# Kernel optimization log

Hardware: AMD Instinct MI355X
Metric: run time of the kernel (lower is better)

Reference implementation:

```python
import jax, jax.numpy as jnp
import numpy as np

D_MODEL = 1024; D_STATE = 128; D_CONV = 4; EXPAND = 2; HEADDIM = 64
D_INNER = EXPAND * D_MODEL          # 2048
NHEADS = D_INNER // HEADDIM         # 32
CONV_DIM = D_INNER + 2 * D_STATE    # 2304 (ngroups=1)
D_IN_PROJ = 2 * D_INNER + 2 * D_STATE + NHEADS  # 4384
B = 2; L = 2048; EPS = 1e-5


def _rmsnorm(x, w):
    return x * jax.lax.rsqrt(jnp.mean(x * x, axis=-1, keepdims=True) + EPS) * w


def _mamba2(x, W_in, conv_w, conv_b, dt_bias, A_log, Dskip, norm_w, W_out):
    # Faithful Mamba2 forward (mamba-ssm defaults: ngroups=1, rmsnorm gated, no proj bias)
    Bb, Ll, _ = x.shape
    zxbcdt = x @ W_in.T                                   # (B,L,D_IN_PROJ)
    z = zxbcdt[..., :D_INNER]
    xBC = zxbcdt[..., D_INNER:D_INNER + CONV_DIM]
    dt = jax.nn.softplus(zxbcdt[..., D_INNER + CONV_DIM:] + dt_bias)  # (B,L,H)
    # depthwise causal conv1d + silu over xBC
    xBC = jnp.transpose(xBC, (0, 2, 1))                   # (B,C,L)
    xBC = jax.lax.conv_general_dilated(xBC, conv_w[:, None, :], (1,), [(D_CONV - 1, 0)],
                                       feature_group_count=CONV_DIM)
    xBC = jax.nn.silu(jnp.transpose(xBC + conv_b[None, :, None], (0, 2, 1)))  # (B,L,C)
    xs = xBC[..., :D_INNER].reshape(Bb, Ll, NHEADS, HEADDIM)
    Bm = xBC[..., D_INNER:D_INNER + D_STATE]              # (B,L,N)
    Cm = xBC[..., D_INNER + D_STATE:]                     # (B,L,N)
    A = -jnp.exp(A_log)                                   # (H,)
    dA = jnp.exp(dt * A)                                  # (B,L,H)

    def step(state, inp):
        dA_t, dt_t, B_t, C_t, x_t = inp
        dBx = jnp.einsum('bh,bn,bhp->bhpn', dt_t, B_t, x_t)
        state = state * dA_t[:, :, None, None] + dBx      # (B,H,P,N)
        return state, jnp.einsum('bhpn,bn->bhp', state, C_t)

    state0 = jnp.zeros((Bb, NHEADS, HEADDIM, D_STATE), x.dtype)
    _, y = jax.lax.scan(step, state0,
                        (jnp.moveaxis(dA, 1, 0), jnp.moveaxis(dt, 1, 0), jnp.moveaxis(Bm, 1, 0),
                         jnp.moveaxis(Cm, 1, 0), jnp.moveaxis(xs, 1, 0)))
    y = jnp.moveaxis(y, 0, 1) + Dskip[None, None, :, None] * xs  # D skip connection
    y = y.reshape(Bb, Ll, D_INNER)
    y = _rmsnorm(y * jax.nn.silu(z), norm_w)              # gated RMSNorm
    return y @ W_out.T                                    # (B,L,D_MODEL)


def setup_inputs() -> dict:
    key = jax.random.key(0)
    ks = jax.random.split(key, 4)

    def nrm(k, shape, s=0.02):
        return jax.random.normal(k, shape, jnp.float32) * s

    def mamba_params(kk):
        k = jax.random.split(kk, 5)
        return dict(W_in=nrm(k[0], (D_IN_PROJ, D_MODEL)),
                    conv_w=nrm(k[1], (CONV_DIM, D_CONV), 0.2),
                    conv_b=jnp.zeros((CONV_DIM,), jnp.float32),
                    dt_bias=jax.random.uniform(k[2], (NHEADS,), jnp.float32, -4.0, -2.0),
                    A_log=jnp.log(jax.random.uniform(k[3], (NHEADS,), jnp.float32, 1.0, 16.0)),
                    D=jnp.ones((NHEADS,), jnp.float32),
                    norm_w=jnp.ones((D_INNER,), jnp.float32),
                    W_out=nrm(k[4], (D_MODEL, D_INNER)))

    pf = mamba_params(ks[1]); pb = mamba_params(ks[2])
    out = {"x": jax.random.normal(ks[0], (B, L, D_MODEL), jnp.float32),
           "norm_weight": jnp.ones((D_MODEL,), jnp.float32)}
    out.update({f"fwd_{k}": v for k, v in pf.items()})
    out.update({f"bwd_{k}": v for k, v in pb.items()})
    out["proj_W"] = nrm(ks[3], (D_MODEL, 2 * D_MODEL))
    out["proj_b"] = jnp.zeros((D_MODEL,), jnp.float32)
    return out


def reference(x, norm_weight,
              fwd_W_in, fwd_conv_w, fwd_conv_b, fwd_dt_bias, fwd_A_log, fwd_D, fwd_norm_w, fwd_W_out,
              bwd_W_in, bwd_conv_w, bwd_conv_b, bwd_dt_bias, bwd_A_log, bwd_D, bwd_norm_w, bwd_W_out,
              proj_W, proj_b):
    residual = x
    xn = _rmsnorm(x, norm_weight)
    y_fwd = _mamba2(xn, fwd_W_in, fwd_conv_w, fwd_conv_b, fwd_dt_bias, fwd_A_log, fwd_D, fwd_norm_w, fwd_W_out)
    y_bwd = jnp.flip(_mamba2(jnp.flip(xn, 1), bwd_W_in, bwd_conv_w, bwd_conv_b, bwd_dt_bias,
                             bwd_A_log, bwd_D, bwd_norm_w, bwd_W_out), 1)
    out = jnp.concatenate([y_fwd, y_bwd], axis=-1) @ proj_W.T + proj_b
    return residual + out
```

## Files before the change

kernel.cpp:

```cpp
#include <hip/hip_runtime.h>
#include <math.h>

#define B_ 2
#define L_ 2048
#define DM 1024
#define DS 128
#define DI 2048
#define NH 32
#define CONVD 2304
#define DIP 4384
#define NPAD 4480
#define EPS_ 1e-5f
#define Q_ 128
#define NC_ 16
#define PT 136

typedef __attribute__((ext_vector_type(8))) short bf16x8;
typedef __attribute__((ext_vector_type(4))) float f32x4;

__device__ __forceinline__ float silu_f(float x) { return x / (1.0f + __expf(-x)); }

__device__ __forceinline__ unsigned short f2bf(float x) {
    union { float f; unsigned u; } v; v.f = x;
    unsigned r = v.u + 0x7fffu + ((v.u >> 16) & 1u);
    return (unsigned short)(r >> 16);
}
__device__ __forceinline__ float bf2f(unsigned short s) {
    union { unsigned u; float f; } v; v.u = ((unsigned)s) << 16; return v.f;
}

__device__ __forceinline__ void gload_lds16(const unsigned short* g, unsigned short* l) {
    __builtin_amdgcn_global_load_lds(
        (const __attribute__((address_space(1))) unsigned int*)g,
        (__attribute__((address_space(3))) unsigned int*)l, 16, 0, 0);
}

__global__ __launch_bounds__(256) void castpad_kernel(
    const float* __restrict__ src, unsigned short* __restrict__ dst, int n_src, int n_dst)
{
    int i = (blockIdx.x * 256 + threadIdx.x) * 4;
    if (i >= n_dst) return;
    ushort4 o;
    if (i < n_src) {
        float4 v = *(const float4*)(src + i);
        o = make_ushort4(f2bf(v.x), f2bf(v.y), f2bf(v.z), f2bf(v.w));
    } else {
        o = make_ushort4(0, 0, 0, 0);
    }
    *(ushort4*)(dst + i) = o;
}

__global__ __launch_bounds__(256) void rmsnorm_kernel(
    const float* __restrict__ x, const float* __restrict__ w, unsigned short* __restrict__ out)
{
    int row = blockIdx.x;
    int t = threadIdx.x;
    const float4* xr = (const float4*)(x + (size_t)row * DM);
    float4 v = xr[t];
    float ss = v.x*v.x + v.y*v.y + v.z*v.z + v.w*v.w;
#pragma unroll
    for (int o = 32; o > 0; o >>= 1) ss += __shfl_down(ss, o, 64);
    __shared__ float red[4];
    if ((t & 63) == 0) red[t >> 6] = ss;
    __syncthreads();
    float tot = red[0] + red[1] + red[2] + red[3];
    float inv = rsqrtf(tot * (1.0f / DM) + EPS_);
    float4 wv = ((const float4*)w)[t];
    ushort4 o4 = make_ushort4(f2bf(v.x * inv * wv.x), f2bf(v.y * inv * wv.y),
                              f2bf(v.z * inv * wv.z), f2bf(v.w * inv * wv.w));
    ((ushort4*)(out + (size_t)row * DM))[t] = o4;
}

__global__ __launch_bounds__(256, 2) void gemm_bf16_kernel(
    const unsigned short* __restrict__ A, const unsigned short* __restrict__ Wt,
    float* __restrict__ C, unsigned short* __restrict__ C16,
    const float* __restrict__ bias, const float* __restrict__ resid,
    int M, int N, int K, int ldc, int col_off, int flipA, int flipOut)
{
    __shared__ unsigned short As[128 * 32];
    __shared__ unsigned short Bs[128 * 32];
    const int tid = threadIdx.x;
    const int lane = tid & 63, wave = tid >> 6;
    const int wr = wave >> 1, wc = wave & 1;
    const int r16 = lane & 15, kg = lane >> 4;
    const int bn0 = blockIdx.x * 128;
    const int bm0 = blockIdx.y * 128;

    f32x4 acc[4][4];
#pragma unroll
    for (int m = 0; m < 4; ++m)
#pragma unroll
        for (int n = 0; n < 4; ++n) { f32x4 z = {0.f, 0.f, 0.f, 0.f}; acc[m][n] = z; }

    for (int k0 = 0; k0 < K; k0 += 32) {
#pragma unroll
        for (int i = 0; i < 2; ++i) {
            int c = wave * 128 + i * 64 + lane;
            int r = c >> 2;
            int kk = (c & 3) << 3;
            int gr = bm0 + r;
            if (flipA) gr ^= (L_ - 1);
            gload_lds16(A + (size_t)gr * K + k0 + kk, As + (size_t)(wave * 128 + i * 64) * 8);
            gload_lds16(Wt + (size_t)(bn0 + r) * K + k0 + kk, Bs + (size_t)(wave * 128 + i * 64) * 8);
        }
        __syncthreads();
        bf16x8 af[4], bfr[4];
        const bf16x8* Ap = (const bf16x8*)As;
        const bf16x8* Bp = (const bf16x8*)Bs;
#pragma unroll
        for (int m = 0; m < 4; ++m) af[m] = Ap[(wr * 64 + m * 16 + r16) * 4 + kg];
#pragma unroll
        for (int n = 0; n < 4; ++n) bfr[n] = Bp[(wc * 64 + n * 16 + r16) * 4 + kg];
#pragma unroll
        for (int m = 0; m < 4; ++m)
#pragma unroll
            for (int n = 0; n < 4; ++n)
                acc[m][n] = __builtin_amdgcn_mfma_f32_16x16x32_bf16(af[m], bfr[n], acc[m][n], 0, 0, 0);
        __syncthreads();
    }

#pragma unroll
    for (int m = 0; m < 4; ++m) {
        int row = bm0 + wr * 64 + m * 16 + kg * 4;
#pragma unroll
        for (int n = 0; n < 4; ++n) {
            int col = bn0 + wc * 64 + n * 16 + r16;
            if (col < N) {
                float bv = bias ? bias[col] : 0.f;
#pragma unroll
                for (int j = 0; j < 4; ++j) {
                    int ro = flipOut ? ((row + j) ^ (L_ - 1)) : (row + j);
                    size_t o = (size_t)ro * ldc + col_off + col;
                    float val = acc[m][n][j] + bv;
                    if (resid) val += resid[o];
                    if (C16) C16[o] = f2bf(val);
                    else     C[o] = val;
                }
            }
        }
    }
}

__global__ __launch_bounds__(256) void convdt_kernel(
    const float* __restrict__ zx, const float* __restrict__ conv_w,
    const float* __restrict__ conv_b, const float* __restrict__ dt_bias,
    const float* __restrict__ A_log,
    float* __restrict__ xs, float* __restrict__ bc,
    float* __restrict__ dtb, float* __restrict__ dab)
{
    int row = blockIdx.x;
    int l = row & (L_ - 1);
    int t = threadIdx.x;
#pragma unroll
    for (int cc = 0; cc < 9; ++cc) {
        int c = t + cc * 256;
        float acc = conv_b[c];
#pragma unroll
        for (int k = 0; k < 4; ++k) {
            int ll = l - 3 + k;
            if (ll >= 0)
                acc = fmaf(conv_w[c * 4 + k], zx[(size_t)(row - 3 + k) * DIP + DI + c], acc);
        }
        float v = silu_f(acc);
        if (c < DI) xs[(size_t)row * DI + c] = v;
        else        bc[(size_t)row * (2 * DS) + (c - DI)] = v;
    }
    if (t < NH) {
        float xv = zx[(size_t)row * DIP + DI + CONVD + t] + dt_bias[t];
        float dt = (xv > 20.f) ? xv : log1pf(__expf(xv));
        float a = -__expf(A_log[t]);
        dtb[row * NH + t] = dt;
        dab[row * NH + t] = dt * a;
    }
}

__global__ __launch_bounds__(256) void chunk_state_kernel(
    const float* __restrict__ xs, const float* __restrict__ bc,
    const float* __restrict__ dtb, const float* __restrict__ dab,
    float* __restrict__ scs, float* __restrict__ la_sum)
{
    int bh = blockIdx.x, c = blockIdx.y;
    int b = bh >> 5, h = bh & 31;
    size_t base = (size_t)b * L_ + (size_t)c * Q_;
    int t = threadIdx.x;
    const int lane = t & 63, wave = t >> 6;
    const int r16 = lane & 15, kg = lane >> 4;
    const int wr = wave >> 1, wc = wave & 1;

    __shared__ unsigned short xwT[64 * PT];
    __shared__ unsigned short BT[128 * PT];
    __shared__ float la[128], w[128];

    if (t < 128) la[t] = dab[(base + t) * NH + h];
    __syncthreads();
#pragma unroll
    for (int off = 1; off < 128; off <<= 1) {
        float v = 0.f;
        if (t < 128 && t >= off) v = la[t - off];
        __syncthreads();
        if (t < 128) la[t] += v;
        __syncthreads();
    }
    float ltot = la[127];
    if (t < 128) w[t] = __expf(ltot - la[t]) * dtb[(base + t) * NH + h];
    if (t == 0) la_sum[bh * NC_ + c] = ltot;
    __syncthreads();

#pragma unroll
    for (int i = 0; i < 8; ++i) {
        int lin4 = i * 256 + t;
        int s = lin4 >> 4, p4 = (lin4 & 15) << 2;
        float4 xv = *(const float4*)&xs[(base + s) * DI + h * 64 + p4];
        float ws = w[s];
        xwT[(p4 + 0) * PT + s] = f2bf(xv.x * ws);
        xwT[(p4 + 1) * PT + s] = f2bf(xv.y * ws);
        xwT[(p4 + 2) * PT + s] = f2bf(xv.z * ws);
        xwT[(p4 + 3) * PT + s] = f2bf(xv.w * ws);
    }
#pragma unroll
    for (int i = 0; i < 16; ++i) {
        int lin4 = i * 256 + t;
        int s = lin4 >> 5, n4 = (lin4 & 31) << 2;
        float4 bv = *(const float4*)&bc[(base + s) * (2 * DS) + n4];
        BT[(n4 + 0) * PT + s] = f2bf(bv.x);
        BT[(n4 + 1) * PT + s] = f2bf(bv.y);
        BT[(n4 + 2) * PT + s] = f2bf(bv.z);
        BT[(n4 + 3) * PT + s] = f2bf(bv.w);
    }
    __syncthreads();

    f32x4 acc[2][4];
#pragma unroll
    for (int m = 0; m < 2; ++m)
#pragma unroll
        for (int n = 0; n < 4; ++n) { f32x4 z = {0.f, 0.f, 0.f, 0.f}; acc[m][n] = z; }

#pragma unroll
    for (int ks = 0; ks < 4; ++ks) {
        bf16x8 af[2], bfr[4];
#pragma unroll
        for (int m = 0; m < 2; ++m)
            af[m] = *(const bf16x8*)&xwT[(wr * 32 + m * 16 + r16) * PT + ks * 32 + kg * 8];
#pragma unroll
        for (int n = 0; n < 4; ++n)
            bfr[n] = *(const bf16x8*)&BT[(wc * 64 + n * 16 + r16) * PT + ks * 32 + kg * 8];
#pragma unroll
        for (int m = 0; m < 2; ++m)
#pragma unroll
            for (int n = 0; n < 4; ++n)
                acc[m][n] = __builtin_amdgcn_mfma_f32_16x16x32_bf16(af[m], bfr[n], acc[m][n], 0, 0, 0);
    }

    float* outp = scs + (size_t)(bh * NC_ + c) * 8192;
#pragma unroll
    for (int m = 0; m < 2; ++m) {
        int p0 = wr * 32 + m * 16 + kg * 4;
#pragma unroll
        for (int n = 0; n < 4; ++n) {
            int nn = wc * 64 + n * 16 + r16;
#pragma unroll
            for (int j = 0; j < 4; ++j)
                outp[(p0 + j) * 128 + nn] = acc[m][n][j];
        }
    }
}

__global__ __launch_bounds__(256) void chunk_seq_kernel(
    float* __restrict__ scs, const float* __restrict__ la_sum)
{
    int bh = blockIdx.x, t = threadIdx.x;
    float S[32];
#pragma unroll
    for (int i = 0; i < 32; ++i) S[i] = 0.f;
    for (int c = 0; c < NC_; ++c) {
        float ef = __expf(la_sum[bh * NC_ + c]);
        float* p = scs + (size_t)(bh * NC_ + c) * 8192;
#pragma unroll
        for (int i = 0; i < 32; ++i) {
            int idx = i * 256 + t;
            float tmp = p[idx];
            p[idx] = S[i];
            S[i] = fmaf(S[i], ef, tmp);
        }
    }
}

__global__ __launch_bounds__(256) void chunk_out_kernel(
    const float* __restrict__ xs, const float* __restrict__ bc,
    const float* __restrict__ dtb, const float* __restrict__ dab,
    const float* __restrict__ scs, const float* __restrict__ Dskip,
    float* __restrict__ ys)
{
    int bh = blockIdx.x, c = blockIdx.y;
    int b = bh >> 5, h = bh & 31;
    size_t base = (size_t)b * L_ + (size_t)c * Q_;
    int t = threadIdx.x;
    const int lane = t & 63, wave = t >> 6;
    const int r16 = lane & 15, kg = lane >> 4;

    __shared__ unsigned short Cb[128 * PT];
    __shared__ unsigned short Bb[128 * PT];
    __shared__ unsigned short xTb[64 * PT];
    __shared__ unsigned short Sinb[64 * PT];
    __shared__ float la[128], dt[128];

    if (t < 128) {
        la[t] = dab[(base + t) * NH + h];
        dt[t] = dtb[(base + t) * NH + h];
    }
    __syncthreads();
#pragma unroll
    for (int off = 1; off < 128; off <<= 1) {
        float v = 0.f;
        if (t < 128 && t >= off) v = la[t - off];
        __syncthreads();
        if (t < 128) la[t] += v;
        __syncthreads();
    }

#pragma unroll
    for (int i = 0; i < 16; ++i) {
        int lin4 = i * 256 + t;
        int s = lin4 >> 5, n4 = (lin4 & 31) << 2;
        float4 bv = *(const float4*)&bc[(base + s) * (2 * DS) + n4];
        float4 cv = *(const float4*)&bc[(base + s) * (2 * DS) + 128 + n4];
        *(ushort4*)&Bb[s * PT + n4] = make_ushort4(f2bf(bv.x), f2bf(bv.y), f2bf(bv.z), f2bf(bv.w));
        *(ushort4*)&Cb[s * PT + n4] = make_ushort4(f2bf(cv.x), f2bf(cv.y), f2bf(cv.z), f2bf(cv.w));
    }
#pragma unroll
    for (int i = 0; i < 8; ++i) {
        int lin4 = i * 256 + t;
        int s = lin4 >> 4, p4 = (lin4 & 15) << 2;
        float4 xv = *(const float4*)&xs[(base + s) * DI + h * 64 + p4];
        xTb[(p4 + 0) * PT + s] = f2bf(xv.x);
        xTb[(p4 + 1) * PT + s] = f2bf(xv.y);
        xTb[(p4 + 2) * PT + s] = f2bf(xv.z);
        xTb[(p4 + 3) * PT + s] = f2bf(xv.w);
    }
    {
        const float* sin_g = scs + (size_t)(bh * NC_ + c) * 8192;
#pragma unroll
        for (int i = 0; i < 8; ++i) {
            int lin4 = i * 256 + t;
            int p = lin4 >> 5, n4 = (lin4 & 31) << 2;
            float4 sv = *(const float4*)&sin_g[p * 128 + n4];
            *(ushort4*)&Sinb[p * PT + n4] = make_ushort4(f2bf(sv.x), f2bf(sv.y), f2bf(sv.z), f2bf(sv.w));
        }
    }
    __syncthreads();

    const int wr = wave >> 1, wc = wave & 1;
    f32x4 acc[4][4];
#pragma unroll
    for (int m = 0; m < 4; ++m)
#pragma unroll
        for (int n = 0; n < 4; ++n) { f32x4 z = {0.f, 0.f, 0.f, 0.f}; acc[m][n] = z; }
    const bool skipq = (wr == 0 && wc == 1);
    if (!skipq) {
#pragma unroll
        for (int ks = 0; ks < 4; ++ks) {
            bf16x8 af[4], bfr[4];
#pragma unroll
            for (int m = 0; m < 4; ++m)
                af[m] = *(const bf16x8*)&Cb[(wr * 64 + m * 16 + r16) * PT + ks * 32 + kg * 8];
#pragma unroll
            for (int n = 0; n < 4; ++n)
                bfr[n] = *(const bf16x8*)&Bb[(wc * 64 + n * 16 + r16) * PT + ks * 32 + kg * 8];
#pragma unroll
            for (int m = 0; m < 4; ++m)
#pragma unroll
                for (int n = 0; n < 4; ++n)
                    acc[m][n] = __builtin_amdgcn_mfma_f32_16x16x32_bf16(af[m], bfr[n], acc[m][n], 0, 0, 0);
        }
    }
    __syncthreads();

#pragma unroll
    for (int m = 0; m < 4; ++m) {
        int t0 = wr * 64 + m * 16 + kg * 4;
#pragma unroll
        for (int n = 0; n < 4; ++n) {
            int sx = wc * 64 + n * 16 + r16;
            float las = la[sx], dts = dt[sx];
#pragma unroll
            for (int j = 0; j < 4; ++j) {
                int tr = t0 + j;
                float v = 0.f;
                if (!skipq && sx <= tr) v = acc[m][n][j] * __expf(la[tr] - las) * dts;
                Bb[tr * PT + sx] = f2bf(v);
            }
        }
    }

    const int wr2 = wave >> 1, wc2 = wave & 1;
    f32x4 acc2[4][2];
#pragma unroll
    for (int m = 0; m < 4; ++m)
#pragma unroll
        for (int n = 0; n < 2; ++n) { f32x4 z = {0.f, 0.f, 0.f, 0.f}; acc2[m][n] = z; }
#pragma unroll
    for (int ks = 0; ks < 4; ++ks) {
        bf16x8 af[4], bfr[2];
#pragma unroll
        for (int m = 0; m < 4; ++m)
            af[m] = *(const bf16x8*)&Cb[(wr2 * 64 + m * 16 + r16) * PT + ks * 32 + kg * 8];
#pragma unroll
        for (int n = 0; n < 2; ++n)
            bfr[n] = *(const bf16x8*)&Sinb[(wc2 * 32 + n * 16 + r16) * PT + ks * 32 + kg * 8];
#pragma unroll
        for (int m = 0; m < 4; ++m)
#pragma unroll
            for (int n = 0; n < 2; ++n)
                acc2[m][n] = __builtin_amdgcn_mfma_f32_16x16x32_bf16(af[m], bfr[n], acc2[m][n], 0, 0, 0);
    }
#pragma unroll
    for (int m = 0; m < 4; ++m) {
        int t0 = wr2 * 64 + m * 16 + kg * 4;
#pragma unroll
        for (int j = 0; j < 4; ++j) {
            float e = __expf(la[t0 + j]);
#pragma unroll
            for (int n = 0; n < 2; ++n) acc2[m][n][j] *= e;
        }
    }
    __syncthreads();

#pragma unroll
    for (int ks = 0; ks < 4; ++ks) {
        bf16x8 af[4], bfr[2];
#pragma unroll
        for (int m = 0; m < 4; ++m)
            af[m] = *(const bf16x8*)&Bb[(wr2 * 64 + m * 16 + r16) * PT + ks * 32 + kg * 8];
#pragma unroll
        for (int n = 0; n < 2; ++n)
            bfr[n] = *(const bf16x8*)&xTb[(wc2 * 32 + n * 16 + r16) * PT + ks * 32 + kg * 8];
#pragma unroll
        for (int m = 0; m < 4; ++m)
#pragma unroll
            for (int n = 0; n < 2; ++n)
                acc2[m][n] = __builtin_amdgcn_mfma_f32_16x16x32_bf16(af[m], bfr[n], acc2[m][n], 0, 0, 0);
    }

    float Dv = Dskip[h];
#pragma unroll
    for (int m = 0; m < 4; ++m) {
        int t0 = wr2 * 64 + m * 16 + kg * 4;
#pragma unroll
        for (int n = 0; n < 2; ++n) {
            int p = wc2 * 32 + n * 16 + r16;
#pragma unroll
            for (int j = 0; j < 4; ++j) {
                int tr = t0 + j;
                float xv = bf2f(xTb[p * PT + tr]);
                ys[(base + tr) * DI + h * 64 + p] = acc2[m][n][j] + Dv * xv;
            }
        }
    }
}

__global__ __launch_bounds__(256) void gate_kernel(
    const float* __restrict__ ys, const float* __restrict__ zx,
    const float* __restrict__ nw, unsigned short* __restrict__ u)
{
    int row = blockIdx.x;
    int t = threadIdx.x;
    const float4* yr = (const float4*)(ys + (size_t)row * DI);
    const float4* zr = (const float4*)(zx + (size_t)row * DIP);
    float g[2][4];
    float ss = 0.f;
#pragma unroll
    for (int it = 0; it < 2; ++it) {
        int i = t + it * 256;
        float4 y4 = yr[i];
        float4 z4 = zr[i];
        float gv;
        gv = y4.x * silu_f(z4.x); g[it][0] = gv; ss += gv * gv;
        gv = y4.y * silu_f(z4.y); g[it][1] = gv; ss += gv * gv;
        gv = y4.z * silu_f(z4.z); g[it][2] = gv; ss += gv * gv;
        gv = y4.w * silu_f(z4.w); g[it][3] = gv; ss += gv * gv;
    }
#pragma unroll
    for (int o = 32; o > 0; o >>= 1) ss += __shfl_down(ss, o, 64);
    __shared__ float red[4];
    if ((t & 63) == 0) red[t >> 6] = ss;
    __syncthreads();
    float tot = red[0] + red[1] + red[2] + red[3];
    float inv = rsqrtf(tot * (1.0f / DI) + EPS_);
#pragma unroll
    for (int it = 0; it < 2; ++it) {
        int i = t + it * 256;
        float4 w4 = ((const float4*)nw)[i];
        ushort4 o4 = make_ushort4(f2bf(g[it][0] * inv * w4.x), f2bf(g[it][1] * inv * w4.y),
                                  f2bf(g[it][2] * inv * w4.z), f2bf(g[it][3] * inv * w4.w));
        ((ushort4*)(u + (size_t)row * DI))[i] = o4;
    }
}

extern "C" void kernel_launch(void* const* d_in, const int* in_sizes, int n_in,
                              void* d_out, int out_size, void* d_ws, size_t ws_size,
                              hipStream_t stream)
{
    (void)in_sizes; (void)n_in; (void)out_size;
    const float* x        = (const float*)d_in[0];
    const float* norm_w   = (const float*)d_in[1];
    const float* Win[2]   = {(const float*)d_in[2],  (const float*)d_in[10]};
    const float* convw[2] = {(const float*)d_in[3],  (const float*)d_in[11]};
    const float* convb[2] = {(const float*)d_in[4],  (const float*)d_in[12]};
    const float* dtbias[2]= {(const float*)d_in[5],  (const float*)d_in[13]};
    const float* Alog[2]  = {(const float*)d_in[6],  (const float*)d_in[14]};
    const float* Dsk[2]   = {(const float*)d_in[7],  (const float*)d_in[15]};
    const float* mnw[2]   = {(const float*)d_in[8],  (const float*)d_in[16]};
    const float* Wout[2]  = {(const float*)d_in[9],  (const float*)d_in[17]};
    const float* projW    = (const float*)d_in[18];
    const float* projb    = (const float*)d_in[19];
    float* out = (float*)d_out;

    const int M = B_ * L_;

    char* base = (char*)d_ws;
    size_t off = 0;
    #define WALLOC(name, type, count) \
        type* name = (type*)(base + off); off = (off + (size_t)(count) * sizeof(type) + 255) & ~(size_t)255;
    WALLOC(xnb,  unsigned short, (size_t)M * DM)
    WALLOC(zx,   float,          (size_t)M * DIP)
    WALLOC(xs,   float,          (size_t)M * DI)
    WALLOC(bcb,  float,          (size_t)M * 2 * DS)
    WALLOC(dtb,  float,          (size_t)M * NH)
    WALLOC(dab,  float,          (size_t)M * NH)
    WALLOC(ysb,  float,          (size_t)M * DI)
    WALLOC(ub,   unsigned short, (size_t)M * DI)
    WALLOC(dbb,  unsigned short, (size_t)M * DI)
    WALLOC(scs,  float,          (size_t)64 * NC_ * 64 * 128)
    WALLOC(lasum, float,         (size_t)64 * NC_)
    WALLOC(winb0, unsigned short, (size_t)NPAD * DM)
    WALLOC(winb1, unsigned short, (size_t)NPAD * DM)
    WALLOC(woutb0, unsigned short, (size_t)DM * DI)
    WALLOC(woutb1, unsigned short, (size_t)DM * DI)
    WALLOC(projwb, unsigned short, (size_t)DM * DI)
    #undef WALLOC
    if (off > ws_size) return;

    unsigned short* winb[2]  = {winb0, winb1};
    unsigned short* woutb[2] = {woutb0, woutb1};

    castpad_kernel<<<(NPAD * DM / 4 + 255) / 256, 256, 0, stream>>>(Win[0], winb0, DIP * DM, NPAD * DM);
    castpad_kernel<<<(NPAD * DM / 4 + 255) / 256, 256, 0, stream>>>(Win[1], winb1, DIP * DM, NPAD * DM);
    castpad_kernel<<<(DM * DI / 4 + 255) / 256, 256, 0, stream>>>(Wout[0], woutb0, DM * DI, DM * DI);
    castpad_kernel<<<(DM * DI / 4 + 255) / 256, 256, 0, stream>>>(Wout[1], woutb1, DM * DI, DM * DI);
    castpad_kernel<<<(DM * DI / 4 + 255) / 256, 256, 0, stream>>>(projW, projwb, DM * DI, DM * DI);

    rmsnorm_kernel<<<M, 256, 0, stream>>>(x, norm_w, xnb);

    for (int d = 0; d < 2; ++d) {
        gemm_bf16_kernel<<<dim3(NPAD / 128, M / 128), 256, 0, stream>>>(
            xnb, winb[d], zx, nullptr, nullptr, nullptr, M, DIP, DM, DIP, 0, d, 0);
        convdt_kernel<<<M, 256, 0, stream>>>(zx, convw[d], convb[d], dtbias[d],
                                             Alog[d], xs, bcb, dtb, dab);
        chunk_state_kernel<<<dim3(64, NC_), 256, 0, stream>>>(xs, bcb, dtb, dab, scs, lasum);
        chunk_seq_kernel<<<64, 256, 0, stream>>>(scs, lasum);
        chunk_out_kernel<<<dim3(64, NC_), 256, 0, stream>>>(xs, bcb, dtb, dab, scs, Dsk[d], ysb);
        gate_kernel<<<M, 256, 0, stream>>>(ysb, zx, mnw[d], ub);
        gemm_bf16_kernel<<<dim3(DM / 128, M / 128), 256, 0, stream>>>(
            ub, woutb[d], nullptr, dbb, nullptr, nullptr, M, DM, DI, 2 * DM, d * DM, 0, d);
    }
    gemm_bf16_kernel<<<dim3(DM / 128, M / 128), 256, 0, stream>>>(
        dbb, projwb, out, nullptr, projb, x, M, DM, 2 * DM, DM, 0, 0, 0);
}
```

Before: 768.9 us.

## Store intermediates in bf16, swizzle GEMM LDS and workgroups, restructure conv

The in-projection GEMM now writes zx as bf16 and routes the dt columns to a separate fp32 buffer. The conv, SSM chunk kernels and gate kernel now read and write bf16 activations (xs, bc, ys), which halves intermediate memory traffic. The GEMM gains an XOR swizzle on the LDS k-groups to reduce bank conflicts and a workgroup remap for better L2 locality. The conv kernel becomes a per-channel sliding window over 64 rows with a separate dt kernel. The cost is extra bf16 rounding of conv outputs and y before the gate.

```diff
diff --git a/kernel.cpp b/kernel.cpp
--- a/kernel.cpp
+++ b/kernel.cpp
@@ -10,6 +10,7 @@
 #define CONVD 2304
 #define DIP 4384
 #define NPAD 4480
+#define DTOFF 4352
 #define EPS_ 1e-5f
 #define Q_ 128
 #define NC_ 16
@@ -73,7 +74,7 @@
 
 __global__ __launch_bounds__(256, 2) void gemm_bf16_kernel(
     const unsigned short* __restrict__ A, const unsigned short* __restrict__ Wt,
-    float* __restrict__ C, unsigned short* __restrict__ C16,
+    float* __restrict__ C, unsigned short* __restrict__ C16, float* __restrict__ Cdt,
     const float* __restrict__ bias, const float* __restrict__ resid,
     int M, int N, int K, int ldc, int col_off, int flipA, int flipOut)
 {
@@ -83,34 +84,42 @@
     const int lane = tid & 63, wave = tid >> 6;
     const int wr = wave >> 1, wc = wave & 1;
     const int r16 = lane & 15, kg = lane >> 4;
-    const int bn0 = blockIdx.x * 128;
-    const int bm0 = blockIdx.y * 128;
+
+    const int gx = gridDim.x;
+    const int nwg = gx * gridDim.y;
+    const int wg = blockIdx.y * gx + blockIdx.x;
+    const int swzg = (wg & 7) * (nwg >> 3) + (wg >> 3);
+    const int bn0 = (swzg % gx) * 128;
+    const int bm0 = (swzg / gx) * 128;
 
     f32x4 acc[4][4];
 #pragma unroll
     for (int m = 0; m < 4; ++m)
 #pragma unroll
         for (int n = 0; n < 4; ++n) { f32x4 z = {0.f, 0.f, 0.f, 0.f}; acc[m][n] = z; }
+
+    const int kswz = kg ^ ((r16 >> 1) & 3);
 
     for (int k0 = 0; k0 < K; k0 += 32) {
 #pragma unroll
         for (int i = 0; i < 2; ++i) {
             int c = wave * 128 + i * 64 + lane;
             int r = c >> 2;
-            int kk = (c & 3) << 3;
+            int ks = c & 3;
+            int ksrc = (ks ^ ((r >> 1) & 3)) << 3;
             int gr = bm0 + r;
             if (flipA) gr ^= (L_ - 1);
-            gload_lds16(A + (size_t)gr * K + k0 + kk, As + (size_t)(wave * 128 + i * 64) * 8);
-            gload_lds16(Wt + (size_t)(bn0 + r) * K + k0 + kk, Bs + (size_t)(wave * 128 + i * 64) * 8);
+            gload_lds16(A + (size_t)gr * K + k0 + ksrc, As + (size_t)(wave * 128 + i * 64) * 8);
+            gload_lds16(Wt + (size_t)(bn0 + r) * K + k0 + ksrc, Bs + (size_t)(wave * 128 + i * 64) * 8);
         }
         __syncthreads();
         bf16x8 af[4], bfr[4];
         const bf16x8* Ap = (const bf16x8*)As;
         const bf16x8* Bp = (const bf16x8*)Bs;
 #pragma unroll
-        for (int m = 0; m < 4; ++m) af[m] = Ap[(wr * 64 + m * 16 + r16) * 4 + kg];
-#pragma unroll
-        for (int n = 0; n < 4; ++n) bfr[n] = Bp[(wc * 64 + n * 16 + r16) * 4 + kg];
+        for (int m = 0; m < 4; ++m) af[m] = Ap[(wr * 64 + m * 16 + r16) * 4 + kswz];
+#pragma unroll
+        for (int n = 0; n < 4; ++n) bfr[n] = Bp[(wc * 64 + n * 16 + r16) * 4 + kswz];
 #pragma unroll
         for (int m = 0; m < 4; ++m)
 #pragma unroll
@@ -133,8 +142,12 @@
                     size_t o = (size_t)ro * ldc + col_off + col;
                     float val = acc[m][n][j] + bv;
                     if (resid) val += resid[o];
-                    if (C16) C16[o] = f2bf(val);
-                    else     C[o] = val;
+                    if (C16) {
+                        if (Cdt && col >= DTOFF) Cdt[(size_t)ro * NH + (col - DTOFF)] = val;
+                        else                     C16[o] = f2bf(val);
+                    } else {
+                        C[o] = val;
+                    }
                 }
             }
         }
@@ -142,40 +155,49 @@
 }
 
 __global__ __launch_bounds__(256) void convdt_kernel(
-    const float* __restrict__ zx, const float* __restrict__ conv_w,
-    const float* __restrict__ conv_b, const float* __restrict__ dt_bias,
-    const float* __restrict__ A_log,
-    float* __restrict__ xs, float* __restrict__ bc,
-    float* __restrict__ dtb, float* __restrict__ dab)
-{
-    int row = blockIdx.x;
-    int l = row & (L_ - 1);
-    int t = threadIdx.x;
-#pragma unroll
-    for (int cc = 0; cc < 9; ++cc) {
-        int c = t + cc * 256;
-        float acc = conv_b[c];
-#pragma unroll
-        for (int k = 0; k < 4; ++k) {
-            int ll = l - 3 + k;
-            if (ll >= 0)
-                acc = fmaf(conv_w[c * 4 + k], zx[(size_t)(row - 3 + k) * DIP + DI + c], acc);
-        }
-        float v = silu_f(acc);
-        if (c < DI) xs[(size_t)row * DI + c] = v;
-        else        bc[(size_t)row * (2 * DS) + (c - DI)] = v;
-    }
-    if (t < NH) {
-        float xv = zx[(size_t)row * DIP + DI + CONVD + t] + dt_bias[t];
-        float dt = (xv > 20.f) ? xv : log1pf(__expf(xv));
-        float a = -__expf(A_log[t]);
-        dtb[row * NH + t] = dt;
-        dab[row * NH + t] = dt * a;
-    }
+    const unsigned short* __restrict__ zxb, const float* __restrict__ conv_w,
+    const float* __restrict__ conv_b,
+    unsigned short* __restrict__ xs16, unsigned short* __restrict__ bc16)
+{
+    int c = blockIdx.x * 256 + threadIdx.x;
+    int r0 = blockIdx.y * 64;
+    float w0 = conv_w[c * 4 + 0], w1 = conv_w[c * 4 + 1];
+    float w2 = conv_w[c * 4 + 2], w3 = conv_w[c * 4 + 3];
+    float bcv = conv_b[c];
+    const unsigned short* src = zxb + DI + c;
+
+    float h0 = 0.f, h1 = 0.f, h2 = 0.f;
+    int l0 = r0 & (L_ - 1);
+    if (l0 >= 3) h0 = bf2f(src[(size_t)(r0 - 3) * DIP]);
+    if (l0 >= 2) h1 = bf2f(src[(size_t)(r0 - 2) * DIP]);
+    if (l0 >= 1) h2 = bf2f(src[(size_t)(r0 - 1) * DIP]);
+
+    for (int j = 0; j < 64; ++j) {
+        size_t row = (size_t)(r0 + j);
+        float cur = bf2f(src[row * DIP]);
+        float a = fmaf(w0, h0, fmaf(w1, h1, fmaf(w2, h2, fmaf(w3, cur, bcv))));
+        float v = silu_f(a);
+        if (c < DI) xs16[row * DI + c] = f2bf(v);
+        else        bc16[row * (2 * DS) + (c - DI)] = f2bf(v);
+        h0 = h1; h1 = h2; h2 = cur;
+    }
+}
+
+__global__ __launch_bounds__(256) void dt_kernel(
+    const float* __restrict__ dtraw, const float* __restrict__ dt_bias,
+    const float* __restrict__ A_log, float* __restrict__ dtb, float* __restrict__ dab)
+{
+    int idx = blockIdx.x * 256 + threadIdx.x;
+    int hh = idx & (NH - 1);
+    float xv = dtraw[idx] + dt_bias[hh];
+    float dt = (xv > 20.f) ? xv : log1pf(__expf(xv));
+    float a = -__expf(A_log[hh]);
+    dtb[idx] = dt;
+    dab[idx] = dt * a;
 }
 
 __global__ __launch_bounds__(256) void chunk_state_kernel(
-    const float* __restrict__ xs, const float* __restrict__ bc,
+    const unsigned short* __restrict__ xs16, const unsigned short* __restrict__ bc16,
     const float* __restrict__ dtb, const float* __restrict__ dab,
     float* __restrict__ scs, float* __restrict__ la_sum)
 {
@@ -207,25 +229,23 @@
     __syncthreads();
 
 #pragma unroll
+    for (int i = 0; i < 4; ++i) {
+        int lin = i * 256 + t;
+        int s = lin >> 3, p8 = (lin & 7) << 3;
+        bf16x8 v = *(const bf16x8*)&xs16[(base + s) * DI + h * 64 + p8];
+        float ws = w[s];
+#pragma unroll
+        for (int j = 0; j < 8; ++j)
+            xwT[(p8 + j) * PT + s] = f2bf(bf2f((unsigned short)v[j]) * ws);
+    }
+#pragma unroll
     for (int i = 0; i < 8; ++i) {
-        int lin4 = i * 256 + t;
-        int s = lin4 >> 4, p4 = (lin4 & 15) << 2;
-        float4 xv = *(const float4*)&xs[(base + s) * DI + h * 64 + p4];
-        float ws = w[s];
-        xwT[(p4 + 0) * PT + s] = f2bf(xv.x * ws);
-        xwT[(p4 + 1) * PT + s] = f2bf(xv.y * ws);
-        xwT[(p4 + 2) * PT + s] = f2bf(xv.z * ws);
-        xwT[(p4 + 3) * PT + s] = f2bf(xv.w * ws);
-    }
-#pragma unroll
-    for (int i = 0; i < 16; ++i) {
-        int lin4 = i * 256 + t;
-        int s = lin4 >> 5, n4 = (lin4 & 31) << 2;
-        float4 bv = *(const float4*)&bc[(base + s) * (2 * DS) + n4];
-        BT[(n4 + 0) * PT + s] = f2bf(bv.x);
-        BT[(n4 + 1) * PT + s] = f2bf(bv.y);
-        BT[(n4 + 2) * PT + s] = f2bf(bv.z);
-        BT[(n4 + 3) * PT + s] = f2bf(bv.w);
+        int lin = i * 256 + t;
+        int s = lin >> 4, n8 = (lin & 15) << 3;
+        bf16x8 v = *(const bf16x8*)&bc16[(base + s) * (2 * DS) + n8];
+#pragma unroll
+        for (int j = 0; j < 8; ++j)
+            BT[(n8 + j) * PT + s] = (unsigned short)v[j];
     }
     __syncthreads();
 
@@ -286,10 +306,10 @@
 }
 
 __global__ __launch_bounds__(256) void chunk_out_kernel(
-    const float* __restrict__ xs, const float* __restrict__ bc,
+    const unsigned short* __restrict__ xs16, const unsigned short* __restrict__ bc16,
     const float* __restrict__ dtb, const float* __restrict__ dab,
     const float* __restrict__ scs, const float* __restrict__ Dskip,
-    float* __restrict__ ys)
+    unsigned short* __restrict__ ys16)
 {
     int bh = blockIdx.x, c = blockIdx.y;
     int b = bh >> 5, h = bh & 31;
@@ -319,23 +339,20 @@
     }
 
 #pragma unroll
-    for (int i = 0; i < 16; ++i) {
-        int lin4 = i * 256 + t;
-        int s = lin4 >> 5, n4 = (lin4 & 31) << 2;
-        float4 bv = *(const float4*)&bc[(base + s) * (2 * DS) + n4];
-        float4 cv = *(const float4*)&bc[(base + s) * (2 * DS) + 128 + n4];
-        *(ushort4*)&Bb[s * PT + n4] = make_ushort4(f2bf(bv.x), f2bf(bv.y), f2bf(bv.z), f2bf(bv.w));
-        *(ushort4*)&Cb[s * PT + n4] = make_ushort4(f2bf(cv.x), f2bf(cv.y), f2bf(cv.z), f2bf(cv.w));
-    }
-#pragma unroll
     for (int i = 0; i < 8; ++i) {
-        int lin4 = i * 256 + t;
-        int s = lin4 >> 4, p4 = (lin4 & 15) << 2;
-        float4 xv = *(const float4*)&xs[(base + s) * DI + h * 64 + p4];
-        xTb[(p4 + 0) * PT + s] = f2bf(xv.x);
-        xTb[(p4 + 1) * PT + s] = f2bf(xv.y);
-        xTb[(p4 + 2) * PT + s] = f2bf(xv.z);
-        xTb[(p4 + 3) * PT + s] = f2bf(xv.w);
+        int lin = i * 256 + t;
+        int s = lin >> 4, n8 = (lin & 15) << 3;
+        *(bf16x8*)&Bb[s * PT + n8] = *(const bf16x8*)&bc16[(base + s) * (2 * DS) + n8];
+        *(bf16x8*)&Cb[s * PT + n8] = *(const bf16x8*)&bc16[(base + s) * (2 * DS) + 128 + n8];
+    }
+#pragma unroll
+    for (int i = 0; i < 4; ++i) {
+        int lin = i * 256 + t;
+        int s = lin >> 3, p8 = (lin & 7) << 3;
+        bf16x8 v = *(const bf16x8*)&xs16[(base + s) * DI + h * 64 + p8];
+#pragma unroll
+        for (int j = 0; j < 8; ++j)
+            xTb[(p8 + j) * PT + s] = (unsigned short)v[j];
     }
     {
         const float* sin_g = scs + (size_t)(bh * NC_ + c) * 8192;
@@ -392,7 +409,6 @@
         }
     }
 
-    const int wr2 = wave >> 1, wc2 = wave & 1;
     f32x4 acc2[4][2];
 #pragma unroll
     for (int m = 0; m < 4; ++m)
@@ -403,10 +419,10 @@
         bf16x8 af[4], bfr[2];
 #pragma unroll
         for (int m = 0; m < 4; ++m)
-            af[m] = *(const bf16x8*)&Cb[(wr2 * 64 + m * 16 + r16) * PT + ks * 32 + kg * 8];
+            af[m] = *(const bf16x8*)&Cb[(wr * 64 + m * 16 + r16) * PT + ks * 32 + kg * 8];
 #pragma unroll
         for (int n = 0; n < 2; ++n)
-            bfr[n] = *(const bf16x8*)&Sinb[(wc2 * 32 + n * 16 + r16) * PT + ks * 32 + kg * 8];
+            bfr[n] = *(const bf16x8*)&Sinb[(wc * 32 + n * 16 + r16) * PT + ks * 32 + kg * 8];
 #pragma unroll
         for (int m = 0; m < 4; ++m)
 #pragma unroll
@@ -415,7 +431,7 @@
     }
 #pragma unroll
     for (int m = 0; m < 4; ++m) {
-        int t0 = wr2 * 64 + m * 16 + kg * 4;
+        int t0 = wr * 64 + m * 16 + kg * 4;
 #pragma unroll
         for (int j = 0; j < 4; ++j) {
             float e = __expf(la[t0 + j]);
@@ -430,10 +446,10 @@
         bf16x8 af[4], bfr[2];
 #pragma unroll
         for (int m = 0; m < 4; ++m)
-            af[m] = *(const bf16x8*)&Bb[(wr2 * 64 + m * 16 + r16) * PT + ks * 32 + kg * 8];
+            af[m] = *(const bf16x8*)&Bb[(wr * 64 + m * 16 + r16) * PT + ks * 32 + kg * 8];
 #pragma unroll
         for (int n = 0; n < 2; ++n)
-            bfr[n] = *(const bf16x8*)&xTb[(wc2 * 32 + n * 16 + r16) * PT + ks * 32 + kg * 8];
+            bfr[n] = *(const bf16x8*)&xTb[(wc * 32 + n * 16 + r16) * PT + ks * 32 + kg * 8];
 #pragma unroll
         for (int m = 0; m < 4; ++m)
 #pragma unroll
@@ -444,40 +460,34 @@
     float Dv = Dskip[h];
 #pragma unroll
     for (int m = 0; m < 4; ++m) {
-        int t0 = wr2 * 64 + m * 16 + kg * 4;
+        int t0 = wr * 64 + m * 16 + kg * 4;
 #pragma unroll
         for (int n = 0; n < 2; ++n) {
-            int p = wc2 * 32 + n * 16 + r16;
+            int p = wc * 32 + n * 16 + r16;
 #pragma unroll
             for (int j = 0; j < 4; ++j) {
                 int tr = t0 + j;
                 float xv = bf2f(xTb[p * PT + tr]);
-                ys[(base + tr) * DI + h * 64 + p] = acc2[m][n][j] + Dv * xv;
+                ys16[(base + tr) * DI + h * 64 + p] = f2bf(acc2[m][n][j] + Dv * xv);
             }
         }
     }
 }
 
 __global__ __launch_bounds__(256) void gate_kernel(
-    const float* __restrict__ ys, const float* __restrict__ zx,
+    const unsigned short* __restrict__ ys16, const unsigned short* __restrict__ zxb,
     const float* __restrict__ nw, unsigned short* __restrict__ u)
 {
     int row = blockIdx.x;
     int t = threadIdx.x;
-    const float4* yr = (const float4*)(ys + (size_t)row * DI);
-    const float4* zr = (const float4*)(zx + (size_t)row * DIP);
-    float g[2][4];
+    bf16x8 yv = *(const bf16x8*)&ys16[(size_t)row * DI + t * 8];
+    bf16x8 zv = *(const bf16x8*)&zxb[(size_t)row * DIP + t * 8];
+    float g[8];
     float ss = 0.f;
 #pragma unroll
-    for (int it = 0; it < 2; ++it) {
-        int i = t + it * 256;
-        float4 y4 = yr[i];
-        float4 z4 = zr[i];
-        float gv;
-        gv = y4.x * silu_f(z4.x); g[it][0] = gv; ss += gv * gv;
-        gv = y4.y * silu_f(z4.y); g[it][1] = gv; ss += gv * gv;
-        gv = y4.z * silu_f(z4.z); g[it][2] = gv; ss += gv * gv;
-        gv = y4.w * silu_f(z4.w); g[it][3] = gv; ss += gv * gv;
+    for (int j = 0; j < 8; ++j) {
+        float gv = bf2f((unsigned short)yv[j]) * silu_f(bf2f((unsigned short)zv[j]));
+        g[j] = gv; ss += gv * gv;
     }
 #pragma unroll
     for (int o = 32; o > 0; o >>= 1) ss += __shfl_down(ss, o, 64);
@@ -486,14 +496,14 @@
     __syncthreads();
     float tot = red[0] + red[1] + red[2] + red[3];
     float inv = rsqrtf(tot * (1.0f / DI) + EPS_);
-#pragma unroll
-    for (int it = 0; it < 2; ++it) {
-        int i = t + it * 256;
-        float4 w4 = ((const float4*)nw)[i];
-        ushort4 o4 = make_ushort4(f2bf(g[it][0] * inv * w4.x), f2bf(g[it][1] * inv * w4.y),
-                                  f2bf(g[it][2] * inv * w4.z), f2bf(g[it][3] * inv * w4.w));
-        ((ushort4*)(u + (size_t)row * DI))[i] = o4;
-    }
+    float4 w0 = *(const float4*)&nw[t * 8];
+    float4 w1 = *(const float4*)&nw[t * 8 + 4];
+    bf16x8 o8;
+    o8[0] = (short)f2bf(g[0] * inv * w0.x); o8[1] = (short)f2bf(g[1] * inv * w0.y);
+    o8[2] = (short)f2bf(g[2] * inv * w0.z); o8[3] = (short)f2bf(g[3] * inv * w0.w);
+    o8[4] = (short)f2bf(g[4] * inv * w1.x); o8[5] = (short)f2bf(g[5] * inv * w1.y);
+    o8[6] = (short)f2bf(g[6] * inv * w1.z); o8[7] = (short)f2bf(g[7] * inv * w1.w);
+    *(bf16x8*)&u[(size_t)row * DI + t * 8] = o8;
 }
 
 extern "C" void kernel_launch(void* const* d_in, const int* in_sizes, int n_in,
@@ -521,17 +531,18 @@
     size_t off = 0;
     #define WALLOC(name, type, count) \
         type* name = (type*)(base + off); off = (off + (size_t)(count) * sizeof(type) + 255) & ~(size_t)255;
-    WALLOC(xnb,  unsigned short, (size_t)M * DM)
-    WALLOC(zx,   float,          (size_t)M * DIP)
-    WALLOC(xs,   float,          (size_t)M * DI)
-    WALLOC(bcb,  float,          (size_t)M * 2 * DS)
-    WALLOC(dtb,  float,          (size_t)M * NH)
-    WALLOC(dab,  float,          (size_t)M * NH)
-    WALLOC(ysb,  float,          (size_t)M * DI)
-    WALLOC(ub,   unsigned short, (size_t)M * DI)
-    WALLOC(dbb,  unsigned short, (size_t)M * DI)
-    WALLOC(scs,  float,          (size_t)64 * NC_ * 64 * 128)
-    WALLOC(lasum, float,         (size_t)64 * NC_)
+    WALLOC(xnb,   unsigned short, (size_t)M * DM)
+    WALLOC(zxb,   unsigned short, (size_t)M * DIP)
+    WALLOC(dtraw, float,          (size_t)M * NH)
+    WALLOC(xs16,  unsigned short, (size_t)M * DI)
+    WALLOC(bc16,  unsigned short, (size_t)M * 2 * DS)
+    WALLOC(dtb,   float,          (size_t)M * NH)
+    WALLOC(dab,   float,          (size_t)M * NH)
+    WALLOC(ys16,  unsigned short, (size_t)M * DI)
+    WALLOC(ub,    unsigned short, (size_t)M * DI)
+    WALLOC(dbb,   unsigned short, (size_t)M * DI)
+    WALLOC(scs,   float,          (size_t)64 * NC_ * 64 * 128)
+    WALLOC(lasum, float,          (size_t)64 * NC_)
     WALLOC(winb0, unsigned short, (size_t)NPAD * DM)
     WALLOC(winb1, unsigned short, (size_t)NPAD * DM)
     WALLOC(woutb0, unsigned short, (size_t)DM * DI)
@@ -553,16 +564,18 @@
 
     for (int d = 0; d < 2; ++d) {
         gemm_bf16_kernel<<<dim3(NPAD / 128, M / 128), 256, 0, stream>>>(
-            xnb, winb[d], zx, nullptr, nullptr, nullptr, M, DIP, DM, DIP, 0, d, 0);
-        convdt_kernel<<<M, 256, 0, stream>>>(zx, convw[d], convb[d], dtbias[d],
-                                             Alog[d], xs, bcb, dtb, dab);
-        chunk_state_kernel<<<dim3(64, NC_), 256, 0, stream>>>(xs, bcb, dtb, dab, scs, lasum);
+            xnb, winb[d], nullptr, zxb, dtraw, nullptr, nullptr,
+            M, DIP, DM, DIP, 0, d, 0);
+        convdt_kernel<<<dim3(9, M / 64), 256, 0, stream>>>(zxb, convw[d], convb[d], xs16, bc16);
+        dt_kernel<<<M * NH / 256, 256, 0, stream>>>(dtraw, dtbias[d], Alog[d], dtb, dab);
+        chunk_state_kernel<<<dim3(64, NC_), 256, 0, stream>>>(xs16, bc16, dtb, dab, scs, lasum);
         chunk_seq_kernel<<<64, 256, 0, stream>>>(scs, lasum);
-        chunk_out_kernel<<<dim3(64, NC_), 256, 0, stream>>>(xs, bcb, dtb, dab, scs, Dsk[d], ysb);
-        gate_kernel<<<M, 256, 0, stream>>>(ysb, zx, mnw[d], ub);
+        chunk_out_kernel<<<dim3(64, NC_), 256, 0, stream>>>(xs16, bc16, dtb, dab, scs, Dsk[d], ys16);
+        gate_kernel<<<M, 256, 0, stream>>>(ys16, zxb, mnw[d], ub);
         gemm_bf16_kernel<<<dim3(DM / 128, M / 128), 256, 0, stream>>>(
-            ub, woutb[d], nullptr, dbb, nullptr, nullptr, M, DM, DI, 2 * DM, d * DM, 0, d);
+            ub, woutb[d], nullptr, dbb, nullptr, nullptr, nullptr,
+            M, DM, DI, 2 * DM, d * DM, 0, d);
     }
     gemm_bf16_kernel<<<dim3(DM / 128, M / 128), 256, 0, stream>>>(
-        dbb, projwb, out, nullptr, projb, x, M, DM, 2 * DM, DM, 0, 0, 0);
-}
+        dbb, projwb, out, nullptr, nullptr, projb, x, M, DM, 2 * DM, DM, 0, 0, 0);
+}
```

New measurement: 708.2 us. 7.9% less time.
